# Kernel tuning notes

Measured on AMD Instinct MI355X. Metric: run time of the kernel, lower is better.

Reference implementation:

```python
import jax, jax.numpy as jnp
import numpy as np

EPS = 1e-5  # BatchNorm2d default eps


def setup_inputs() -> dict:
    key = jax.random.key(0)
    k1, k2, k3, k4 = jax.random.split(key, 4)
    B, C, S, E = 2, 512, 256, 512  # C == E is required by the module's math
    x = jax.random.normal(k1, (B, C, S, E), dtype=jnp.float32)
    Q = jax.random.normal(k2, (E, E), dtype=jnp.float32)
    K = jax.random.normal(k3, (E, E), dtype=jnp.float32)
    V = jax.random.normal(k4, (E, E), dtype=jnp.float32)
    return {"x": x, "Q": Q, "K": K, "V": V}


def reference(x, Q, K, V):
    # BatchNorm2d(affine=False), training-mode batch stats over (B, H, W)
    mean = jnp.mean(x, axis=(0, 2, 3), keepdims=True)
    var = jnp.var(x, axis=(0, 2, 3), keepdims=True)  # biased, matches torch normalization
    xn = (x - mean) * jax.lax.rsqrt(var + EPS)

    divisor = jnp.sqrt(jnp.asarray(x.shape[-1], dtype=x.dtype))
    q = jnp.einsum('bcse,ef->bcsf', xn, Q)
    k = jnp.einsum('bcse,ef->bcsf', xn, K)
    v = jnp.einsum('bcse,ef->bcsf', xn, V)

    # scores: [B, C, S, S]
    prod = jnp.einsum('bcsf,bctf->bcst', q, k) / divisor
    # nn.Softmax2d softmaxes over the CHANNEL dim (axis 1)
    sm = jax.nn.softmax(prod, axis=1)
    attention = jnp.einsum('bcst,bctf->bcsf', sm, v)
    # dropout is identity in eval/reference mode; residual since E_in == E_out
    return attention + xn
```

## Files before the change

kernel.cpp:

```cpp
#include <hip/hip_runtime.h>
#include <hip/hip_bf16.h>
#include <cstdio>

#define Bn 2
#define Cn 512
#define Sn 256
#define En 512

typedef __attribute__((ext_vector_type(8))) short bf16x8;
typedef __attribute__((ext_vector_type(4))) float f32x4;

static constexpr size_t PROD_B = (1ull << 20);
static constexpr size_t V_B    = PROD_B + (256ull << 20);
static constexpr size_t ATH_B  = V_B + (256ull << 20);
static constexpr size_t ATL_B  = ATH_B + (512ull << 10);
static constexpr size_t VT_B   = ATL_B + (512ull << 10);
static constexpr size_t XNH_B  = VT_B + (512ull << 10);
static constexpr size_t XNL_B  = XNH_B + (256ull << 20);
static constexpr size_t WS_BIG = XNL_B + (256ull << 20);
static constexpr size_t SMT_B  = XNL_B;

__device__ __forceinline__ unsigned short f2bf(float f) {
  union { __hip_bfloat16 h; unsigned short u; } cv;
  cv.h = __float2bfloat16(f);
  return cv.u;
}
__device__ __forceinline__ float bf2f(unsigned short u) {
  union { unsigned int i; float f; } cv;
  cv.i = ((unsigned int)u) << 16;
  return cv.f;
}
__device__ __forceinline__ void split2(float v, unsigned short& h, unsigned short& l) {
  h = f2bf(v);
  l = f2bf(v - bf2f(h));
}
__device__ __forceinline__ int swzc(int row, int col) {
  return row * 64 + ((col & 3) | ((col & 60) ^ ((row & 7) << 3)));
}
__device__ __forceinline__ bf16x8 ldfrag(const unsigned short* arr, int row, int ks, int lane) {
  const int byte = (ks * 64 + ((lane >> 4) << 4)) ^ ((row & 7) << 4);
  return *(const bf16x8*)((const char*)(arr + (size_t)row * 64) + byte);
}
__device__ __forceinline__ f32x4 MFMA(bf16x8 a, bf16x8 b, f32x4 c) {
  return __builtin_amdgcn_mfma_f32_16x16x32_bf16(a, b, c, 0, 0, 0);
}
__device__ __forceinline__ void glds16(const void* g, void* l) {
  __builtin_amdgcn_global_load_lds(
      (const __attribute__((address_space(1))) unsigned int*)g,
      (__attribute__((address_space(3))) unsigned int*)l, 16, 0, 0);
}
__device__ __forceinline__ void stage_tile(const unsigned short* g, unsigned short* l,
                                           int nbytes, int wid, int lane, int nwaves) {
  const char* gb = (const char*)g;
  char* lb = (char*)l;
  for (int j = wid; j < (nbytes >> 10); j += nwaves)
    glds16(gb + j * 1024 + lane * 16, lb + j * 1024);
}

__global__ void k1_stats(const float* __restrict__ x, float* __restrict__ ws) {
  const int c = blockIdx.x, tid = threadIdx.x;
  const float4* p0 = (const float4*)(x + (size_t)c * (Sn * En));
  const float4* p1 = (const float4*)(x + (size_t)(Cn + c) * (Sn * En));
  float s1 = 0.f, s2 = 0.f;
  for (int i = tid; i < (Sn * En / 4); i += 256) {
    float4 a = p0[i], b = p1[i];
    s1 += (a.x + a.y) + (a.z + a.w) + (b.x + b.y) + (b.z + b.w);
    s2 += (a.x * a.x + a.y * a.y) + (a.z * a.z + a.w * a.w) +
          (b.x * b.x + b.y * b.y) + (b.z * b.z + b.w * b.w);
  }
  __shared__ float r1[256], r2[256];
  r1[tid] = s1; r2[tid] = s2;
  __syncthreads();
  for (int off = 128; off > 0; off >>= 1) {
    if (tid < off) { r1[tid] += r1[tid + off]; r2[tid] += r2[tid + off]; }
    __syncthreads();
  }
  if (tid == 0) {
    const float n = (float)(2 * Sn * En);
    float mean = r1[0] / n;
    float var = r2[0] / n - mean * mean;
    ws[c] = mean;
    ws[512 + c] = 1.0f / sqrtf(var + 1e-5f);
  }
}

__global__ void kA(const float* __restrict__ Q, const float* __restrict__ K,
                   const float* __restrict__ V, unsigned short* __restrict__ ATh,
                   unsigned short* __restrict__ ATl, unsigned short* __restrict__ VT) {
  const int f = blockIdx.x, tid = threadIdx.x;
  __shared__ float Kf[512];
  for (int i = tid; i < 512; i += 256) Kf[i] = K[(size_t)f * 512 + i];
  __syncthreads();
  const int fr64 = f & 63;
  const size_t atbase = ((size_t)(f >> 6) * 8) * 4096 + (size_t)fr64 * 64;
  const size_t vtbase = ((size_t)(f >> 7) * 8) * 8192 + (size_t)(f & 127) * 64;
#pragma unroll
  for (int half = 0; half < 2; ++half) {
    const int e = tid + half * 256;
    const float* Qe = Q + (size_t)e * 512;
    float acc = 0.f;
    for (int t = 0; t < 512; t += 4) {
      float4 q = *(const float4*)(Qe + t);
      acc += q.x * Kf[t] + q.y * Kf[t + 1] + q.z * Kf[t + 2] + q.w * Kf[t + 3];
    }
    unsigned short h, l;
    split2(acc, h, l);
    const int et = e >> 6, ec = e & 63;
    const int swa = (ec & 3) | ((ec & 60) ^ ((fr64 & 7) << 3));
    ATh[atbase + (size_t)et * 4096 + swa] = h;
    ATl[atbase + (size_t)et * 4096 + swa] = l;
    const int swv = (ec & 3) | ((ec & 60) ^ ((f & 7) << 3));
    VT[vtbase + (size_t)et * 8192 + swv] = f2bf(V[(size_t)e * 512 + f]);
  }
}

__global__ void kxn(const float* __restrict__ x, const float* __restrict__ ws,
                    unsigned short* __restrict__ XNh, unsigned short* __restrict__ XNl) {
  const int bid = blockIdx.x;
  const int bc = bid >> 1, half = bid & 1;
  const int c = bc & 511;
  const float mean = ws[c], rstd = ws[512 + c];
  const float* xb = x + (size_t)bc * 131072 + (size_t)half * 128 * 512;
  const int tid = threadIdx.x;
#pragma unroll 4
  for (int i = 0; i < 64; ++i) {
    const int g = tid + i * 256;
    const int r = g >> 7, c4 = g & 127;
    const float4 xv = *(const float4*)(xb + (size_t)r * 512 + c4 * 4);
    ushort4 hv, lv;
    split2((xv.x - mean) * rstd, hv.x, lv.x);
    split2((xv.y - mean) * rstd, hv.y, lv.y);
    split2((xv.z - mean) * rstd, hv.z, lv.z);
    split2((xv.w - mean) * rstd, hv.w, lv.w);
    const int et = c4 >> 4, colt4 = c4 & 15;
    const int row = half * 128 + r;
    const size_t idx = ((size_t)(bc * 8 + et) * 256 + row) * 64 +
                       ((colt4 * 4) ^ ((row & 7) << 3));
    *(ushort4*)&XNh[idx] = hv;
    *(ushort4*)&XNl[idx] = lv;
  }
}

__launch_bounds__(256)
__global__ void kv_proj(const unsigned short* __restrict__ VT,
                        const unsigned short* __restrict__ XNh_g,
                        unsigned short* __restrict__ vT_out) {
  __shared__ unsigned short BUF[2][16384];
  const int bid = blockIdx.x;
  const int L = (bid & 7) * 1024 + (bid >> 3);
  const int bc = L >> 3;
  const int fq = (L >> 1) & 3;
  const int th = L & 1;
  const int f0 = fq * 128, t0 = th * 128;
  const int tid = threadIdx.x, w = tid >> 6, lane = tid & 63;

  f32x4 acc[2][8];
#pragma unroll
  for (int i = 0; i < 2; ++i)
#pragma unroll
    for (int j = 0; j < 8; ++j) acc[i][j] = (f32x4){0.f, 0.f, 0.f, 0.f};

  stage_tile(VT + ((size_t)fq * 8 + 0) * 8192, &BUF[0][0], 16384, w, lane, 4);
  stage_tile(XNh_g + ((size_t)(bc * 8 + 0) * 256 + t0) * 64, &BUF[0][8192], 16384, w, lane, 4);
  __syncthreads();
#pragma unroll 1
  for (int et = 0; et < 8; ++et) {
    if (et < 7) {
      const int b = (et + 1) & 1;
      stage_tile(VT + ((size_t)fq * 8 + et + 1) * 8192, &BUF[b][0], 16384, w, lane, 4);
      stage_tile(XNh_g + ((size_t)(bc * 8 + et + 1) * 256 + t0) * 64, &BUF[b][8192],
                 16384, w, lane, 4);
    }
    const unsigned short* cb = &BUF[et & 1][0];
#pragma unroll
    for (int ks = 0; ks < 2; ++ks) {
      bf16x8 a0 = ldfrag(cb, w * 32 + (lane & 15), ks, lane);
      bf16x8 a1 = ldfrag(cb, w * 32 + 16 + (lane & 15), ks, lane);
#pragma unroll
      for (int ct = 0; ct < 8; ++ct) {
        bf16x8 b = ldfrag(cb + 8192, ct * 16 + (lane & 15), ks, lane);
        acc[0][ct] = MFMA(a0, b, acc[0][ct]);
        acc[1][ct] = MFMA(a1, b, acc[1][ct]);
      }
    }
    __syncthreads();
  }
#pragma unroll
  for (int rt = 0; rt < 2; ++rt)
#pragma unroll
    for (int ct = 0; ct < 8; ++ct)
#pragma unroll
      for (int r = 0; r < 4; ++r) {
        const int f = f0 + w * 32 + rt * 16 + (lane >> 4) * 4 + r;
        const int t = t0 + ct * 16 + (lane & 15);
        const size_t idx = (((size_t)bc * 4 + (f >> 7)) * 4 + (t >> 6)) * 8192 +
                           (size_t)(f & 127) * 64 +
                           ((t & 3) | ((t & 60) ^ ((f & 7) << 3)));
        vT_out[idx] = f2bf(acc[rt][ct][r]);
      }
}

__launch_bounds__(512)
__global__ void kscores(const unsigned short* __restrict__ ATh_g,
                        const unsigned short* __restrict__ ATl_g,
                        const unsigned short* __restrict__ XNh_g,
                        const unsigned short* __restrict__ XNl_g,
                        float* __restrict__ prod) {
  __shared__ unsigned short BUF[2][24576];
  __shared__ unsigned short Yh[128 * 64], Yl[128 * 64];
  const int bid = blockIdx.x;
  const int L = (bid & 7) * 256 + (bid >> 3);
  const int bc = L >> 1, half = L & 1;
  float* prodc = prod + (size_t)bc * 65536 + (size_t)half * 128 * 256;
  const int tid = threadIdx.x, w = tid >> 6, lane = tid & 63;

  f32x4 accz[16];
#pragma unroll
  for (int i = 0; i < 16; ++i) accz[i] = (f32x4){0.f, 0.f, 0.f, 0.f};
  f32x4 accy[4];

  auto stage_slot = [&](int m, int b) {
    const int ft = m / 10, sub = m - ft * 10;
    unsigned short* dst = &BUF[b][0];
    if (sub < 8) {
      stage_tile(XNh_g + ((size_t)(bc * 8 + sub) * 256 + half * 128) * 64, dst,
                 16384, w, lane, 8);
      stage_tile(XNl_g + ((size_t)(bc * 8 + sub) * 256 + half * 128) * 64, dst + 8192,
                 16384, w, lane, 8);
      stage_tile(ATh_g + ((size_t)ft * 8 + sub) * 4096, dst + 16384, 8192, w, lane, 8);
      stage_tile(ATl_g + ((size_t)ft * 8 + sub) * 4096, dst + 20480, 8192, w, lane, 8);
    } else {
      const int th = sub - 8;
      stage_tile(XNh_g + ((size_t)(bc * 8 + ft) * 256 + th * 128) * 64, dst,
                 16384, w, lane, 8);
      stage_tile(XNl_g + ((size_t)(bc * 8 + ft) * 256 + th * 128) * 64, dst + 8192,
                 16384, w, lane, 8);
    }
  };

  stage_slot(0, 0);
  __syncthreads();

#pragma unroll 1
  for (int m = 0; m < 80; ++m) {
    const int sub = m % 10;
    if (m < 79) stage_slot(m + 1, (m + 1) & 1);
    const unsigned short* cb = &BUF[m & 1][0];
    if (sub == 0) {
#pragma unroll
      for (int i = 0; i < 4; ++i) accy[i] = (f32x4){0.f, 0.f, 0.f, 0.f};
    }
    if (sub < 8) {
#pragma unroll
      for (int ks = 0; ks < 2; ++ks) {
        bf16x8 ah = ldfrag(cb, w * 16 + (lane & 15), ks, lane);
        bf16x8 al = ldfrag(cb + 8192, w * 16 + (lane & 15), ks, lane);
#pragma unroll
        for (int fc = 0; fc < 4; ++fc) {
          bf16x8 bh = ldfrag(cb + 16384, fc * 16 + (lane & 15), ks, lane);
          bf16x8 bl = ldfrag(cb + 20480, fc * 16 + (lane & 15), ks, lane);
          accy[fc] = MFMA(ah, bh, accy[fc]);
          accy[fc] = MFMA(ah, bl, accy[fc]);
          accy[fc] = MFMA(al, bh, accy[fc]);
        }
      }
      if (sub == 7) {
#pragma unroll
        for (int fc = 0; fc < 4; ++fc)
#pragma unroll
          for (int r = 0; r < 4; ++r) {
            const int row = w * 16 + (lane >> 4) * 4 + r;
            const int col = fc * 16 + (lane & 15);
            unsigned short h, l;
            split2(accy[fc][r], h, l);
            const int idx = swzc(row, col);
            Yh[idx] = h;
            Yl[idx] = l;
          }
      }
    } else if (sub == 8) {
#pragma unroll
      for (int ks = 0; ks < 2; ++ks) {
        bf16x8 ah = ldfrag(Yh, w * 16 + (lane & 15), ks, lane);
        bf16x8 al = ldfrag(Yl, w * 16 + (lane & 15), ks, lane);
#pragma unroll
        for (int ct = 0; ct < 8; ++ct) {
          bf16x8 bh = ldfrag(cb, ct * 16 + (lane & 15), ks, lane);
          bf16x8 bl = ldfrag(cb + 8192, ct * 16 + (lane & 15), ks, lane);
          accz[ct] = MFMA(ah, bh, accz[ct]);
          accz[ct] = MFMA(ah, bl, accz[ct]);
          accz[ct] = MFMA(al, bh, accz[ct]);
        }
      }
    } else {
#pragma unroll
      for (int ks = 0; ks < 2; ++ks) {
        bf16x8 ah = ldfrag(Yh, w * 16 + (lane & 15), ks, lane);
        bf16x8 al = ldfrag(Yl, w * 16 + (lane & 15), ks, lane);
#pragma unroll
        for (int ct = 0; ct < 8; ++ct) {
          bf16x8 bh = ldfrag(cb, ct * 16 + (lane & 15), ks, lane);
          bf16x8 bl = ldfrag(cb + 8192, ct * 16 + (lane & 15), ks, lane);
          accz[8 + ct] = MFMA(ah, bh, accz[8 + ct]);
          accz[8 + ct] = MFMA(ah, bl, accz[8 + ct]);
          accz[8 + ct] = MFMA(al, bh, accz[8 + ct]);
        }
      }
    }
    __syncthreads();
  }

  const float scale = 0.044194173824159216f;
#pragma unroll
  for (int th = 0; th < 2; ++th)
#pragma unroll
    for (int ct = 0; ct < 8; ++ct)
#pragma unroll
      for (int r = 0; r < 4; ++r) {
        const int row = w * 16 + (lane >> 4) * 4 + r;
        prodc[(size_t)row * 256 + th * 128 + ct * 16 + (lane & 15)] =
            accz[th * 8 + ct][r] * scale;
      }
}

__launch_bounds__(512)
__global__ void k3_softmax(const float* __restrict__ prodf, unsigned short* __restrict__ smT) {
  const int bid = blockIdx.x;
  const int b = bid >> 8, s = bid & 255;
  const int tid = threadIdx.x;
  const int t = tid & 255, ch = tid >> 8;
  const float* __restrict__ p =
      prodf + (size_t)b * (512ull * 65536) + (size_t)s * 256 + t + (size_t)ch * 256 * 65536;
  float m = -3.4e38f, sum = 0.f;
#pragma unroll 4
  for (int cc = 0; cc < 256; ++cc) {
    const float v = p[(size_t)cc * 65536];
    if (v > m) { sum *= __expf(m - v); m = v; }
    sum += __expf(v - m);
  }
  __shared__ float Ms[2][256], Ss[2][256];
  Ms[ch][t] = m; Ss[ch][t] = sum;
  __syncthreads();
  const float mo = Ms[ch ^ 1][t], so = Ss[ch ^ 1][t];
  const float mm = fmaxf(m, mo);
  const float inv = 1.0f / (sum * __expf(m - mm) + so * __expf(mo - mm));
  const int sh = s >> 7, r = s & 127, kt = t >> 6, col = t & 63;
  const int cidx = r * 64 + ((col & 3) | ((col & 60) ^ ((r & 7) << 3)));
  const size_t tbase = ((size_t)b * 512 + ch * 256) * 2 + sh;
#pragma unroll 4
  for (int cc = 0; cc < 256; ++cc) {
    const float ev = __expf(p[(size_t)cc * 65536] - mm) * inv;
    smT[((tbase + (size_t)cc * 2) * 4 + kt) * 8192 + cidx] = f2bf(ev);
  }
}

__launch_bounds__(256)
__global__ void k4_pv(const float* __restrict__ x, const unsigned short* __restrict__ vT,
                      const float* __restrict__ ws, const unsigned short* __restrict__ smT,
                      float* __restrict__ out) {
  __shared__ unsigned short BUF[2][16384];
  const int bid = blockIdx.x;
  const int L = (bid & 7) * 1024 + (bid >> 3);
  const int bc = L >> 3;
  const int sh = (L >> 2) & 1;
  const int fh = L & 3;
  const int c = bc & 511;
  const float mean = ws[c], rstd = ws[512 + c];
  const int s0 = sh * 128, f0 = fh * 128;
  const int tid = threadIdx.x, w = tid >> 6, lane = tid & 63;

  f32x4 acc[2][8];
#pragma unroll
  for (int i = 0; i < 2; ++i)
#pragma unroll
    for (int j = 0; j < 8; ++j) acc[i][j] = (f32x4){0.f, 0.f, 0.f, 0.f};

  stage_tile(smT + (((size_t)bc * 2 + sh) * 4 + 0) * 8192, &BUF[0][0], 16384, w, lane, 4);
  stage_tile(vT + (((size_t)bc * 4 + fh) * 4 + 0) * 8192, &BUF[0][8192], 16384, w, lane, 4);
  __syncthreads();
#pragma unroll 1
  for (int kt = 0; kt < 4; ++kt) {
    if (kt < 3) {
      const int b = (kt + 1) & 1;
      stage_tile(smT + (((size_t)bc * 2 + sh) * 4 + kt + 1) * 8192, &BUF[b][0],
                 16384, w, lane, 4);
      stage_tile(vT + (((size_t)bc * 4 + fh) * 4 + kt + 1) * 8192, &BUF[b][8192],
                 16384, w, lane, 4);
    }
    const unsigned short* cb = &BUF[kt & 1][0];
#pragma unroll
    for (int ks = 0; ks < 2; ++ks) {
      bf16x8 a0 = ldfrag(cb, w * 32 + (lane & 15), ks, lane);
      bf16x8 a1 = ldfrag(cb, w * 32 + 16 + (lane & 15), ks, lane);
#pragma unroll
      for (int ct = 0; ct < 8; ++ct) {
        bf16x8 b = ldfrag(cb + 8192, ct * 16 + (lane & 15), ks, lane);
        acc[0][ct] = MFMA(a0, b, acc[0][ct]);
        acc[1][ct] = MFMA(a1, b, acc[1][ct]);
      }
    }
    __syncthreads();
  }
#pragma unroll
  for (int rt = 0; rt < 2; ++rt)
#pragma unroll
    for (int ct = 0; ct < 8; ++ct)
#pragma unroll
      for (int r = 0; r < 4; ++r) {
        const int srow = s0 + w * 32 + rt * 16 + (lane >> 4) * 4 + r;
        const int fcol = f0 + ct * 16 + (lane & 15);
        const size_t oi = (size_t)bc * 131072 + (size_t)srow * 512 + fcol;
        out[oi] = acc[rt][ct][r] + (x[oi] - mean) * rstd;
      }
}

extern "C" void kernel_launch(void* const* d_in, const int* in_sizes, int n_in,
                              void* d_out, int out_size, void* d_ws, size_t ws_size,
                              hipStream_t stream) {
  const float* x = (const float*)d_in[0];
  const float* Q = (const float*)d_in[1];
  const float* K = (const float*)d_in[2];
  const float* V = (const float*)d_in[3];
  float* out = (float*)d_out;
  float* ws = (float*)d_ws;
  float* prodf = (float*)((char*)d_ws + PROD_B);
  unsigned short* vT   = (unsigned short*)((char*)d_ws + V_B);
  unsigned short* ATh  = (unsigned short*)((char*)d_ws + ATH_B);
  unsigned short* ATl  = (unsigned short*)((char*)d_ws + ATL_B);
  unsigned short* VTm  = (unsigned short*)((char*)d_ws + VT_B);
  unsigned short* XNh  = (unsigned short*)((char*)d_ws + XNH_B);
  unsigned short* XNl  = (unsigned short*)((char*)d_ws + XNL_B);
  unsigned short* smT  = (unsigned short*)((char*)d_ws + SMT_B);
  if (ws_size < WS_BIG) {
    fprintf(stderr, "kernel_launch: ws_size %zu < needed %zu — expect corruption\n",
            ws_size, WS_BIG);
  }
  k1_stats<<<dim3(512), dim3(256), 0, stream>>>(x, ws);
  kA<<<dim3(512), dim3(256), 0, stream>>>(Q, K, V, ATh, ATl, VTm);
  kxn<<<dim3(2048), dim3(256), 0, stream>>>(x, ws, XNh, XNl);
  kv_proj<<<dim3(8192), dim3(256), 0, stream>>>(VTm, XNh, vT);
  kscores<<<dim3(2048), dim3(512), 0, stream>>>(ATh, ATl, XNh, XNl, prodf);
  k3_softmax<<<dim3(512), dim3(512), 0, stream>>>(prodf, smT);
  k4_pv<<<dim3(8192), dim3(256), 0, stream>>>(x, vT, ws, smT, out);
}
```

Before: 2.076 ms.

## Pipeline kscores with four-slot LDS ring and split hi/lo staging

Replaces the double-buffered per-step staging in the scores kernel with a four-slot LDS ring in which the high and low bf16 halves are staged and consumed in separate phases. Explicit vmcnt waits with raw barriers keep several global-to-LDS loads in flight while the MFMA work runs, and s_setprio raises priority during compute. The first GEMM is fully unrolled per ft tile instead of using modulo branching. The aim is to hide load latency behind compute, at the cost of fragile hand-counted wait counts and more LDS use, which may lower occupancy.

```diff
diff --git a/kernel.cpp b/kernel.cpp
--- a/kernel.cpp
+++ b/kernel.cpp
@@ -37,6 +37,9 @@
 __device__ __forceinline__ int swzc(int row, int col) {
   return row * 64 + ((col & 3) | ((col & 60) ^ ((row & 7) << 3)));
 }
+__device__ __forceinline__ int swz8(int row, int c4) {
+  return row * 64 + ((((c4 * 8) ^ ((row & 7) << 4))) >> 1);
+}
 __device__ __forceinline__ bf16x8 ldfrag(const unsigned short* arr, int row, int ks, int lane) {
   const int byte = (ks * 64 + ((lane >> 4) << 4)) ^ ((row & 7) << 4);
   return *(const bf16x8*)((const char*)(arr + (size_t)row * 64) + byte);
@@ -56,6 +59,14 @@
   for (int j = wid; j < (nbytes >> 10); j += nwaves)
     glds16(gb + j * 1024 + lane * 16, lb + j * 1024);
 }
+
+#define WAITB(N)                                                   \
+  do {                                                             \
+    asm volatile("s_waitcnt vmcnt(" #N ")" ::: "memory");          \
+    asm volatile("s_waitcnt lgkmcnt(0)" ::: "memory");             \
+    __builtin_amdgcn_s_barrier();                                  \
+    __builtin_amdgcn_sched_barrier(0);                             \
+  } while (0)
 
 __global__ void k1_stats(const float* __restrict__ x, float* __restrict__ ws) {
   const int c = blockIdx.x, tid = threadIdx.x;
@@ -206,8 +217,12 @@
                         const unsigned short* __restrict__ XNh_g,
                         const unsigned short* __restrict__ XNl_g,
                         float* __restrict__ prod) {
-  __shared__ unsigned short BUF[2][24576];
-  __shared__ unsigned short Yh[128 * 64], Yl[128 * 64];
+  __shared__ unsigned short RING[57344];
+  __shared__ unsigned short Yh[8192], Yl[8192];
+  unsigned short* const S0 = RING;
+  unsigned short* const S1 = RING + 12288;
+  unsigned short* const S2 = RING + 28672;
+  unsigned short* const S3 = RING + 40960;
   const int bid = blockIdx.x;
   const int L = (bid & 7) * 256 + (bid >> 3);
   const int bc = L >> 1, half = L & 1;
@@ -218,96 +233,126 @@
 #pragma unroll
   for (int i = 0; i < 16; ++i) accz[i] = (f32x4){0.f, 0.f, 0.f, 0.f};
   f32x4 accy[4];
-
-  auto stage_slot = [&](int m, int b) {
-    const int ft = m / 10, sub = m - ft * 10;
-    unsigned short* dst = &BUF[b][0];
-    if (sub < 8) {
-      stage_tile(XNh_g + ((size_t)(bc * 8 + sub) * 256 + half * 128) * 64, dst,
-                 16384, w, lane, 8);
-      stage_tile(XNl_g + ((size_t)(bc * 8 + sub) * 256 + half * 128) * 64, dst + 8192,
-                 16384, w, lane, 8);
-      stage_tile(ATh_g + ((size_t)ft * 8 + sub) * 4096, dst + 16384, 8192, w, lane, 8);
-      stage_tile(ATl_g + ((size_t)ft * 8 + sub) * 4096, dst + 20480, 8192, w, lane, 8);
-    } else {
-      const int th = sub - 8;
-      stage_tile(XNh_g + ((size_t)(bc * 8 + ft) * 256 + th * 128) * 64, dst,
-                 16384, w, lane, 8);
-      stage_tile(XNl_g + ((size_t)(bc * 8 + ft) * 256 + th * 128) * 64, dst + 8192,
-                 16384, w, lane, 8);
-    }
-  };
-
-  stage_slot(0, 0);
-  __syncthreads();
+  bf16x8 ahold[2];
+
+  auto stA = [&](int ftx, int et, unsigned short* sl) {
+    stage_tile(XNh_g + ((size_t)(bc * 8 + et) * 256 + half * 128) * 64, sl, 16384, w, lane, 8);
+    stage_tile(ATh_g + ((size_t)ftx * 8 + et) * 4096, sl + 8192, 8192, w, lane, 8);
+  };
+  auto stB = [&](int ftx, int et, unsigned short* sl) {
+    stage_tile(XNl_g + ((size_t)(bc * 8 + et) * 256 + half * 128) * 64, sl, 16384, w, lane, 8);
+    stage_tile(ATl_g + ((size_t)ftx * 8 + et) * 4096, sl + 8192, 8192, w, lane, 8);
+    stage_tile(ATh_g + ((size_t)ftx * 8 + et) * 4096, sl + 12288, 8192, w, lane, 8);
+  };
+  auto st2h = [&](int ftx, int th, unsigned short* sl) {
+    stage_tile(XNh_g + ((size_t)(bc * 8 + ftx) * 256 + th * 128) * 64, sl, 16384, w, lane, 8);
+  };
+  auto st2l = [&](int ftx, int th, unsigned short* sl) {
+    stage_tile(XNl_g + ((size_t)(bc * 8 + ftx) * 256 + th * 128) * 64, sl, 16384, w, lane, 8);
+  };
+  auto cpA = [&](const unsigned short* sl) {
+    __builtin_amdgcn_s_setprio(1);
+#pragma unroll
+    for (int ks = 0; ks < 2; ++ks) {
+      ahold[ks] = ldfrag(sl, w * 16 + (lane & 15), ks, lane);
+#pragma unroll
+      for (int fc = 0; fc < 4; ++fc) {
+        bf16x8 bh = ldfrag(sl + 8192, fc * 16 + (lane & 15), ks, lane);
+        accy[fc] = MFMA(ahold[ks], bh, accy[fc]);
+      }
+    }
+    __builtin_amdgcn_s_setprio(0);
+  };
+  auto cpB = [&](const unsigned short* sl) {
+    __builtin_amdgcn_s_setprio(1);
+#pragma unroll
+    for (int ks = 0; ks < 2; ++ks) {
+      bf16x8 al = ldfrag(sl, w * 16 + (lane & 15), ks, lane);
+#pragma unroll
+      for (int fc = 0; fc < 4; ++fc) {
+        bf16x8 bl = ldfrag(sl + 8192, fc * 16 + (lane & 15), ks, lane);
+        bf16x8 bh = ldfrag(sl + 12288, fc * 16 + (lane & 15), ks, lane);
+        accy[fc] = MFMA(ahold[ks], bl, accy[fc]);
+        accy[fc] = MFMA(al, bh, accy[fc]);
+      }
+    }
+    __builtin_amdgcn_s_setprio(0);
+  };
+  auto cp2A = [&](const unsigned short* sl, int zo) {
+    __builtin_amdgcn_s_setprio(1);
+#pragma unroll
+    for (int ks = 0; ks < 2; ++ks) {
+      bf16x8 a2h = ldfrag(Yh, w * 16 + (lane & 15), ks, lane);
+      bf16x8 a2l = ldfrag(Yl, w * 16 + (lane & 15), ks, lane);
+#pragma unroll
+      for (int ct = 0; ct < 8; ++ct) {
+        bf16x8 bh = ldfrag(sl, ct * 16 + (lane & 15), ks, lane);
+        accz[zo + ct] = MFMA(a2h, bh, accz[zo + ct]);
+        accz[zo + ct] = MFMA(a2l, bh, accz[zo + ct]);
+      }
+    }
+    __builtin_amdgcn_s_setprio(0);
+  };
+  auto cp2B = [&](const unsigned short* sl, int zo) {
+    __builtin_amdgcn_s_setprio(1);
+#pragma unroll
+    for (int ks = 0; ks < 2; ++ks) {
+      bf16x8 a2h = ldfrag(Yh, w * 16 + (lane & 15), ks, lane);
+#pragma unroll
+      for (int ct = 0; ct < 8; ++ct) {
+        bf16x8 bl = ldfrag(sl, ct * 16 + (lane & 15), ks, lane);
+        accz[zo + ct] = MFMA(a2h, bl, accz[zo + ct]);
+      }
+    }
+    __builtin_amdgcn_s_setprio(0);
+  };
+  auto ywrite = [&]() {
+#pragma unroll
+    for (int fc = 0; fc < 4; ++fc)
+#pragma unroll
+      for (int r = 0; r < 4; ++r) {
+        const int row = w * 16 + (lane >> 4) * 4 + r;
+        const int col = fc * 16 + (lane & 15);
+        unsigned short h, l;
+        split2(accy[fc][r], h, l);
+        const int idx = swzc(row, col);
+        Yh[idx] = h;
+        Yl[idx] = l;
+      }
+  };
+
+  stA(0, 0, S0);
+  stB(0, 0, S1);
+  stA(0, 1, S2);
 
 #pragma unroll 1
-  for (int m = 0; m < 80; ++m) {
-    const int sub = m % 10;
-    if (m < 79) stage_slot(m + 1, (m + 1) & 1);
-    const unsigned short* cb = &BUF[m & 1][0];
-    if (sub == 0) {
-#pragma unroll
-      for (int i = 0; i < 4; ++i) accy[i] = (f32x4){0.f, 0.f, 0.f, 0.f};
-    }
-    if (sub < 8) {
-#pragma unroll
-      for (int ks = 0; ks < 2; ++ks) {
-        bf16x8 ah = ldfrag(cb, w * 16 + (lane & 15), ks, lane);
-        bf16x8 al = ldfrag(cb + 8192, w * 16 + (lane & 15), ks, lane);
-#pragma unroll
-        for (int fc = 0; fc < 4; ++fc) {
-          bf16x8 bh = ldfrag(cb + 16384, fc * 16 + (lane & 15), ks, lane);
-          bf16x8 bl = ldfrag(cb + 20480, fc * 16 + (lane & 15), ks, lane);
-          accy[fc] = MFMA(ah, bh, accy[fc]);
-          accy[fc] = MFMA(ah, bl, accy[fc]);
-          accy[fc] = MFMA(al, bh, accy[fc]);
-        }
-      }
-      if (sub == 7) {
-#pragma unroll
-        for (int fc = 0; fc < 4; ++fc)
-#pragma unroll
-          for (int r = 0; r < 4; ++r) {
-            const int row = w * 16 + (lane >> 4) * 4 + r;
-            const int col = fc * 16 + (lane & 15);
-            unsigned short h, l;
-            split2(accy[fc][r], h, l);
-            const int idx = swzc(row, col);
-            Yh[idx] = h;
-            Yl[idx] = l;
-          }
-      }
-    } else if (sub == 8) {
-#pragma unroll
-      for (int ks = 0; ks < 2; ++ks) {
-        bf16x8 ah = ldfrag(Yh, w * 16 + (lane & 15), ks, lane);
-        bf16x8 al = ldfrag(Yl, w * 16 + (lane & 15), ks, lane);
-#pragma unroll
-        for (int ct = 0; ct < 8; ++ct) {
-          bf16x8 bh = ldfrag(cb, ct * 16 + (lane & 15), ks, lane);
-          bf16x8 bl = ldfrag(cb + 8192, ct * 16 + (lane & 15), ks, lane);
-          accz[ct] = MFMA(ah, bh, accz[ct]);
-          accz[ct] = MFMA(ah, bl, accz[ct]);
-          accz[ct] = MFMA(al, bh, accz[ct]);
-        }
-      }
-    } else {
-#pragma unroll
-      for (int ks = 0; ks < 2; ++ks) {
-        bf16x8 ah = ldfrag(Yh, w * 16 + (lane & 15), ks, lane);
-        bf16x8 al = ldfrag(Yl, w * 16 + (lane & 15), ks, lane);
-#pragma unroll
-        for (int ct = 0; ct < 8; ++ct) {
-          bf16x8 bh = ldfrag(cb, ct * 16 + (lane & 15), ks, lane);
-          bf16x8 bl = ldfrag(cb + 8192, ct * 16 + (lane & 15), ks, lane);
-          accz[8 + ct] = MFMA(ah, bh, accz[8 + ct]);
-          accz[8 + ct] = MFMA(ah, bl, accz[8 + ct]);
-          accz[8 + ct] = MFMA(al, bh, accz[8 + ct]);
-        }
-      }
-    }
-    __syncthreads();
+  for (int ft = 0; ft < 8; ++ft) {
+#pragma unroll
+    for (int i = 0; i < 4; ++i) accy[i] = (f32x4){0.f, 0.f, 0.f, 0.f};
+    WAITB(7); stB(ft, 1, S3);  cpA(S0);
+    WAITB(7); stA(ft, 2, S0);  cpB(S1);
+    WAITB(7); stB(ft, 2, S1);  cpA(S2);
+    WAITB(7); stA(ft, 3, S2);  cpB(S3);
+    WAITB(7); stB(ft, 3, S3);  cpA(S0);
+    WAITB(7); stA(ft, 4, S0);  cpB(S1);
+    WAITB(7); stB(ft, 4, S1);  cpA(S2);
+    WAITB(7); stA(ft, 5, S2);  cpB(S3);
+    WAITB(7); stB(ft, 5, S3);  cpA(S0);
+    WAITB(7); stA(ft, 6, S0);  cpB(S1);
+    WAITB(7); stB(ft, 6, S1);  cpA(S2);
+    WAITB(7); stA(ft, 7, S2);  cpB(S3);
+    WAITB(7); stB(ft, 7, S3);  cpA(S0);
+    WAITB(7); st2h(ft, 0, S0); cpB(S1);
+    WAITB(6); st2l(ft, 0, S1); cpA(S2);
+    WAITB(4); st2h(ft, 1, S2); cpB(S3); ywrite();
+    WAITB(4); st2l(ft, 1, S3); cp2A(S0, 0);
+    WAITB(4); if (ft < 7) stA(ft + 1, 0, S0); cp2B(S1, 0);
+    if (ft < 7) { WAITB(5); stB(ft + 1, 0, S1); }
+    else        { WAITB(2); }
+    cp2A(S2, 8);
+    if (ft < 7) { WAITB(7); stA(ft + 1, 1, S2); }
+    else        { WAITB(0); }
+    cp2B(S3, 8);
   }
 
   const float scale = 0.044194173824159216f;
```

Result: slower. 2.189 ms (+5.4%).

## Restructure kscores staging: direct global A-fragments, smaller LDS, per-wave Y buffers

Applied to the files above, without the earlier changes.

The scores kernel no longer stages the xn row tiles for phase 1 in shared memory. Each wave loads its A fragments straight from global memory, and only the AT and xn-transposed tiles are staged, in smaller 64-row chunks. The Y intermediate now lives in a per-wave buffer, and waves_per_eu(4) is requested, both to cut LDS use and raise occupancy. The trade-off is more global loads sitting on the MFMA critical path, more barriers per tile, and register pressure from the waves-per-EU hint.

```diff
diff --git a/kernel.cpp b/kernel.cpp
--- a/kernel.cpp
+++ b/kernel.cpp
@@ -201,126 +201,121 @@
 }
 
 __launch_bounds__(512)
+__attribute__((amdgpu_waves_per_eu(4)))
 __global__ void kscores(const unsigned short* __restrict__ ATh_g,
                         const unsigned short* __restrict__ ATl_g,
                         const unsigned short* __restrict__ XNh_g,
                         const unsigned short* __restrict__ XNl_g,
                         float* __restrict__ prod) {
-  __shared__ unsigned short BUF[2][24576];
-  __shared__ unsigned short Yh[128 * 64], Yl[128 * 64];
+  __shared__ unsigned short STG[2][8192];
+  __shared__ unsigned short YS[8][2048];
   const int bid = blockIdx.x;
   const int L = (bid & 7) * 256 + (bid >> 3);
   const int bc = L >> 1, half = L & 1;
   float* prodc = prod + (size_t)bc * 65536 + (size_t)half * 128 * 256;
   const int tid = threadIdx.x, w = tid >> 6, lane = tid & 63;
+  const int lr = lane & 15, lk = lane >> 4;
+
+  const int arow = half * 128 + w * 16 + lr;
+  const unsigned short* xnh_row = XNh_g + ((size_t)bc * 8 * 256 + arow) * 64;
+  const unsigned short* xnl_row = XNl_g + ((size_t)bc * 8 * 256 + arow) * 64;
+  const int ac0 = (lk * 8) ^ ((arow & 7) << 3);
+  const int ac1 = (32 + lk * 8) ^ ((arow & 7) << 3);
 
   f32x4 accz[16];
 #pragma unroll
   for (int i = 0; i < 16; ++i) accz[i] = (f32x4){0.f, 0.f, 0.f, 0.f};
   f32x4 accy[4];
-
-  auto stage_slot = [&](int m, int b) {
-    const int ft = m / 10, sub = m - ft * 10;
-    unsigned short* dst = &BUF[b][0];
-    if (sub < 8) {
-      stage_tile(XNh_g + ((size_t)(bc * 8 + sub) * 256 + half * 128) * 64, dst,
-                 16384, w, lane, 8);
-      stage_tile(XNl_g + ((size_t)(bc * 8 + sub) * 256 + half * 128) * 64, dst + 8192,
-                 16384, w, lane, 8);
-      stage_tile(ATh_g + ((size_t)ft * 8 + sub) * 4096, dst + 16384, 8192, w, lane, 8);
-      stage_tile(ATl_g + ((size_t)ft * 8 + sub) * 4096, dst + 20480, 8192, w, lane, 8);
-    } else {
-      const int th = sub - 8;
-      stage_tile(XNh_g + ((size_t)(bc * 8 + ft) * 256 + th * 128) * 64, dst,
-                 16384, w, lane, 8);
-      stage_tile(XNl_g + ((size_t)(bc * 8 + ft) * 256 + th * 128) * 64, dst + 8192,
-                 16384, w, lane, 8);
-    }
+  unsigned short* const ys = YS[w];
+
+  auto stAT = [&](int ftx, int et, int p) {
+    stage_tile(ATh_g + ((size_t)ftx * 8 + et) * 4096, STG[p], 8192, w, lane, 8);
+    stage_tile(ATl_g + ((size_t)ftx * 8 + et) * 4096, STG[p] + 4096, 8192, w, lane, 8);
   };
-
-  stage_slot(0, 0);
+  auto stXT = [&](int ftx, int tq, int p) {
+    stage_tile(XNh_g + ((size_t)(bc * 8 + ftx) * 256 + tq * 64) * 64, STG[p], 8192, w, lane, 8);
+    stage_tile(XNl_g + ((size_t)(bc * 8 + ftx) * 256 + tq * 64) * 64, STG[p] + 4096, 8192, w, lane, 8);
+  };
+  auto ph1 = [&](int et, int p) {
+    const bf16x8 ah0 = *(const bf16x8*)(xnh_row + (size_t)et * 16384 + ac0);
+    const bf16x8 al0 = *(const bf16x8*)(xnl_row + (size_t)et * 16384 + ac0);
+    const bf16x8 ah1 = *(const bf16x8*)(xnh_row + (size_t)et * 16384 + ac1);
+    const bf16x8 al1 = *(const bf16x8*)(xnl_row + (size_t)et * 16384 + ac1);
+#pragma unroll
+    for (int fc = 0; fc < 4; ++fc) {
+      bf16x8 bh0 = ldfrag(STG[p], fc * 16 + lr, 0, lane);
+      bf16x8 bl0 = ldfrag(STG[p] + 4096, fc * 16 + lr, 0, lane);
+      accy[fc] = MFMA(ah0, bh0, accy[fc]);
+      accy[fc] = MFMA(ah0, bl0, accy[fc]);
+      accy[fc] = MFMA(al0, bh0, accy[fc]);
+      bf16x8 bh1 = ldfrag(STG[p], fc * 16 + lr, 1, lane);
+      bf16x8 bl1 = ldfrag(STG[p] + 4096, fc * 16 + lr, 1, lane);
+      accy[fc] = MFMA(ah1, bh1, accy[fc]);
+      accy[fc] = MFMA(ah1, bl1, accy[fc]);
+      accy[fc] = MFMA(al1, bh1, accy[fc]);
+    }
+  };
+  auto ph2 = [&](int z0, int p) {
+#pragma unroll
+    for (int ks = 0; ks < 2; ++ks) {
+      bf16x8 yh = ldfrag(ys, lr, ks, lane);
+      bf16x8 yl = ldfrag(ys + 1024, lr, ks, lane);
+#pragma unroll
+      for (int j = 0; j < 4; ++j) {
+        bf16x8 bh = ldfrag(STG[p], j * 16 + lr, ks, lane);
+        bf16x8 bl = ldfrag(STG[p] + 4096, j * 16 + lr, ks, lane);
+        accz[z0 + j] = MFMA(yh, bh, accz[z0 + j]);
+        accz[z0 + j] = MFMA(yh, bl, accz[z0 + j]);
+        accz[z0 + j] = MFMA(yl, bh, accz[z0 + j]);
+      }
+    }
+  };
+  auto ywrite = [&]() {
+#pragma unroll
+    for (int fc = 0; fc < 4; ++fc)
+#pragma unroll
+      for (int r = 0; r < 4; ++r) {
+        const int row = lk * 4 + r;
+        const int col = fc * 16 + lr;
+        unsigned short h, l;
+        split2(accy[fc][r], h, l);
+        const int idx = swzc(row, col);
+        ys[idx] = h;
+        ys[1024 + idx] = l;
+      }
+  };
+
+  stAT(0, 0, 0);
   __syncthreads();
 
 #pragma unroll 1
-  for (int m = 0; m < 80; ++m) {
-    const int sub = m % 10;
-    if (m < 79) stage_slot(m + 1, (m + 1) & 1);
-    const unsigned short* cb = &BUF[m & 1][0];
-    if (sub == 0) {
-#pragma unroll
-      for (int i = 0; i < 4; ++i) accy[i] = (f32x4){0.f, 0.f, 0.f, 0.f};
-    }
-    if (sub < 8) {
-#pragma unroll
-      for (int ks = 0; ks < 2; ++ks) {
-        bf16x8 ah = ldfrag(cb, w * 16 + (lane & 15), ks, lane);
-        bf16x8 al = ldfrag(cb + 8192, w * 16 + (lane & 15), ks, lane);
-#pragma unroll
-        for (int fc = 0; fc < 4; ++fc) {
-          bf16x8 bh = ldfrag(cb + 16384, fc * 16 + (lane & 15), ks, lane);
-          bf16x8 bl = ldfrag(cb + 20480, fc * 16 + (lane & 15), ks, lane);
-          accy[fc] = MFMA(ah, bh, accy[fc]);
-          accy[fc] = MFMA(ah, bl, accy[fc]);
-          accy[fc] = MFMA(al, bh, accy[fc]);
-        }
-      }
-      if (sub == 7) {
-#pragma unroll
-        for (int fc = 0; fc < 4; ++fc)
-#pragma unroll
-          for (int r = 0; r < 4; ++r) {
-            const int row = w * 16 + (lane >> 4) * 4 + r;
-            const int col = fc * 16 + (lane & 15);
-            unsigned short h, l;
-            split2(accy[fc][r], h, l);
-            const int idx = swzc(row, col);
-            Yh[idx] = h;
-            Yl[idx] = l;
-          }
-      }
-    } else if (sub == 8) {
-#pragma unroll
-      for (int ks = 0; ks < 2; ++ks) {
-        bf16x8 ah = ldfrag(Yh, w * 16 + (lane & 15), ks, lane);
-        bf16x8 al = ldfrag(Yl, w * 16 + (lane & 15), ks, lane);
-#pragma unroll
-        for (int ct = 0; ct < 8; ++ct) {
-          bf16x8 bh = ldfrag(cb, ct * 16 + (lane & 15), ks, lane);
-          bf16x8 bl = ldfrag(cb + 8192, ct * 16 + (lane & 15), ks, lane);
-          accz[ct] = MFMA(ah, bh, accz[ct]);
-          accz[ct] = MFMA(ah, bl, accz[ct]);
-          accz[ct] = MFMA(al, bh, accz[ct]);
-        }
-      }
-    } else {
-#pragma unroll
-      for (int ks = 0; ks < 2; ++ks) {
-        bf16x8 ah = ldfrag(Yh, w * 16 + (lane & 15), ks, lane);
-        bf16x8 al = ldfrag(Yl, w * 16 + (lane & 15), ks, lane);
-#pragma unroll
-        for (int ct = 0; ct < 8; ++ct) {
-          bf16x8 bh = ldfrag(cb, ct * 16 + (lane & 15), ks, lane);
-          bf16x8 bl = ldfrag(cb + 8192, ct * 16 + (lane & 15), ks, lane);
-          accz[8 + ct] = MFMA(ah, bh, accz[8 + ct]);
-          accz[8 + ct] = MFMA(ah, bl, accz[8 + ct]);
-          accz[8 + ct] = MFMA(al, bh, accz[8 + ct]);
-        }
-      }
-    }
-    __syncthreads();
+  for (int ft = 0; ft < 8; ++ft) {
+#pragma unroll
+    for (int i = 0; i < 4; ++i) accy[i] = (f32x4){0.f, 0.f, 0.f, 0.f};
+    stAT(ft, 1, 1);                 ph1(0, 0); __syncthreads();
+    stAT(ft, 2, 0);                 ph1(1, 1); __syncthreads();
+    stAT(ft, 3, 1);                 ph1(2, 0); __syncthreads();
+    stAT(ft, 4, 0);                 ph1(3, 1); __syncthreads();
+    stAT(ft, 5, 1);                 ph1(4, 0); __syncthreads();
+    stAT(ft, 6, 0);                 ph1(5, 1); __syncthreads();
+    stAT(ft, 7, 1);                 ph1(6, 0); __syncthreads();
+    stXT(ft, 0, 0);                 ph1(7, 1); __syncthreads();
+    ywrite();
+    stXT(ft, 1, 1);                 ph2(0, 0);  __syncthreads();
+    stXT(ft, 2, 0);                 ph2(4, 1);  __syncthreads();
+    stXT(ft, 3, 1);                 ph2(8, 0);  __syncthreads();
+    if (ft < 7) stAT(ft + 1, 0, 0); ph2(12, 1); __syncthreads();
   }
 
   const float scale = 0.044194173824159216f;
 #pragma unroll
-  for (int th = 0; th < 2; ++th)
-#pragma unroll
-    for (int ct = 0; ct < 8; ++ct)
-#pragma unroll
-      for (int r = 0; r < 4; ++r) {
-        const int row = w * 16 + (lane >> 4) * 4 + r;
-        prodc[(size_t)row * 256 + th * 128 + ct * 16 + (lane & 15)] =
-            accz[th * 8 + ct][r] * scale;
-      }
+  for (int i = 0; i < 16; ++i)
+#pragma unroll
+    for (int r = 0; r < 4; ++r) {
+      const int row = w * 16 + lk * 4 + r;
+      const int col = (i >> 2) * 64 + (i & 3) * 16 + lr;
+      prodc[(size_t)row * 256 + col] = accz[i][r] * scale;
+    }
 }
 
 __launch_bounds__(512)
```

After: 2.345 ms. +12.9%, slower.
